# Performance work log

Hardware: AMD Instinct MI355X
Metric: run time of the kernel (lower is better)

The kernel has to match this reference:

```python
import jax, jax.numpy as jnp
import numpy as np

N = 4096          # N_TARGET_NODES (node count == feature dim)
E = 262144        # number of directed edges (avg degree 64)


def setup_inputs() -> dict:
    key = jax.random.key(0)
    k1, k2, k3, k4 = jax.random.split(key, 4)
    x = jax.random.normal(k1, (N, N), dtype=jnp.float32)
    edge_index = jax.random.randint(k2, (2, E), 0, N, dtype=jnp.int32)
    # scale weights so sigmoid inputs are O(1)
    W1 = jax.random.normal(k3, (N, N), dtype=jnp.float32) * (1.0 / np.sqrt(N))
    b1 = jnp.zeros((N,), dtype=jnp.float32)
    W2 = jax.random.normal(k4, (N, 1), dtype=jnp.float32) * (1.0 / np.sqrt(N))
    b2 = jnp.zeros((1,), dtype=jnp.float32)
    return {"x": x, "edge_index": edge_index, "W1": W1, "b1": b1, "W2": W2, "b2": b2}


def _gcn_conv(x, edge_index, W, b):
    """PyG GCNConv: h = D^{-1/2}(A+I)D^{-1/2} (x W) + b, edge weights = 1."""
    n = x.shape[0]
    h = x @ W                                   # [n, out]
    loop = jnp.arange(n, dtype=edge_index.dtype)
    src = jnp.concatenate([edge_index[0], loop])  # add self loops
    dst = jnp.concatenate([edge_index[1], loop])
    deg = jax.ops.segment_sum(jnp.ones_like(src, dtype=h.dtype), dst, num_segments=n)
    dinv = jnp.where(deg > 0, jax.lax.rsqrt(deg), 0.0)
    norm = dinv[src] * dinv[dst]                # [E+n]
    msg = h[src] * norm[:, None]                # gather + scale
    out = jax.ops.segment_sum(msg, dst, num_segments=n)  # scatter-add at targets
    return out + b


def reference(x, edge_index, W1, b1, W2, b2):
    # torch.squeeze(x) is a no-op for 2-D x
    x1 = jax.nn.sigmoid(_gcn_conv(x, edge_index, W1, b1))
    # F.dropout in eval mode is identity (deterministic reference)
    x2 = jax.nn.sigmoid(_gcn_conv(x1, edge_index, W2, b2))
    return x2  # [N, 1]
```

## Files before the change

kernel.cpp:

```cpp
#include <hip/hip_runtime.h>


typedef __attribute__((ext_vector_type(8))) short bf16x8;
typedef __attribute__((ext_vector_type(4))) float f32x4;

#define NN 4096
#define NT 64

__device__ __forceinline__ unsigned f2bf(float f) {
  unsigned u = __float_as_uint(f);
  return (u + 0x7FFFu + ((u >> 16) & 1u)) >> 16;
}

#define GLDS(g, l) __builtin_amdgcn_global_load_lds(                      \
    (const __attribute__((address_space(1))) void*)(g),                   \
    (__attribute__((address_space(3))) void*)(l), 16, 0, 0)


__global__ void init_deg_kernel(float* deg) {
  int v = blockIdx.x * 256 + threadIdx.x;
  if (v < NN) deg[v] = 1.0f;
}

__global__ void count_deg_kernel(const int* __restrict__ dst, int E, float* deg) {
  int e = blockIdx.x * 256 + threadIdx.x;
  if (e < E) atomicAdd(&deg[dst[e]], 1.0f);
}

__global__ void dinv_kernel(const float* __restrict__ deg, float* __restrict__ dinv) {
  int v = blockIdx.x * 256 + threadIdx.x;
  if (v < NN) dinv[v] = rsqrtf(deg[v]);
}

__global__ void diag_bf16_kernel(const float* __restrict__ dinv, unsigned short* __restrict__ Sbf) {
  int v = blockIdx.x * 256 + threadIdx.x;
  if (v < NN) { float d = dinv[v]; Sbf[(size_t)v * NN + v] = (unsigned short)f2bf(d * d); }
}

__global__ void scatter_bf16_kernel(const int* __restrict__ src, const int* __restrict__ dst,
                                    int E, const float* __restrict__ dinv,
                                    unsigned int* __restrict__ Sw) {
  int e = blockIdx.x * 256 + threadIdx.x;
  if (e >= E) return;
  int s = src[e], d = dst[e];
  float val = dinv[s] * dinv[d];
  size_t idx = (size_t)d * NN + s;
  unsigned int* p = Sw + (idx >> 1);
  const bool hi = (idx & 1) != 0;
  unsigned old = *p, assumed;
  do {
    assumed = old;
    unsigned short cur = hi ? (unsigned short)(assumed >> 16) : (unsigned short)(assumed & 0xFFFFu);
    float f = __uint_as_float(((unsigned)cur) << 16) + val;
    unsigned short nb = (unsigned short)f2bf(f);
    unsigned nw = hi ? ((assumed & 0x0000FFFFu) | ((unsigned)nb << 16))
                     : ((assumed & 0xFFFF0000u) | (unsigned)nb);
    old = atomicCAS(p, assumed, nw);
  } while (old != assumed);
}


__global__ void cast_kernel(const float* __restrict__ in, unsigned short* __restrict__ out, int n) {
  int i = (blockIdx.x * 256 + threadIdx.x) * 8;
  if (i >= n) return;
  const float4* p = (const float4*)(in + i);
  float4 a = p[0], b = p[1];
  uint4 o;
  o.x = f2bf(a.x) | (f2bf(a.y) << 16);
  o.y = f2bf(a.z) | (f2bf(a.w) << 16);
  o.z = f2bf(b.x) | (f2bf(b.y) << 16);
  o.w = f2bf(b.z) | (f2bf(b.w) << 16);
  *(uint4*)(out + i) = o;
}

__global__ void transpose_cast_kernel(const float* __restrict__ W, unsigned short* __restrict__ WT) {
  __shared__ float tile[64][65];
  const int tid = threadIdx.x;
  const int bx = blockIdx.x * 64, by = blockIdx.y * 64;
  const int tx = tid & 63, ty = tid >> 6;
#pragma unroll
  for (int i = 0; i < 64; i += 4)
    tile[ty + i][tx] = W[(size_t)(by + ty + i) * NN + bx + tx];
  __syncthreads();
  const int wtx = tid & 15, wty = tid >> 4;
#pragma unroll
  for (int i = 0; i < 64; i += 16) {
    int r = wty + i;
    ushort4 v;
    v.x = (unsigned short)f2bf(tile[4 * wtx + 0][r]);
    v.y = (unsigned short)f2bf(tile[4 * wtx + 1][r]);
    v.z = (unsigned short)f2bf(tile[4 * wtx + 2][r]);
    v.w = (unsigned short)f2bf(tile[4 * wtx + 3][r]);
    *(ushort4*)(WT + (size_t)(bx + r) * NN + by + 4 * wtx) = v;
  }
}


template <int EPI>
__global__ __launch_bounds__(512, 2) void gemm256_kernel(
    const unsigned short* __restrict__ A, const unsigned short* __restrict__ BT,
    unsigned short* __restrict__ C, const float* __restrict__ bias,
    const float* __restrict__ W2, float* __restrict__ h2) {
  __shared__ __align__(16) char smem[131072];
  const int tid = threadIdx.x;
  const int lane = tid & 63, wid = tid >> 6;
  const int wr = wid >> 2, wc = wid & 3;

  const int bid = blockIdx.x;
  const int swz = (bid & 7) * 32 + (bid >> 3);
  const int rowBase = (swz >> 4) * 256;
  const int colBase = (swz & 15) * 256;

  const int srow = tid >> 3;
  const int scolb = ((tid & 7) << 4) ^ ((srow & 7) << 4);
  const unsigned short* pA = A + (size_t)(rowBase + srow) * NN + (scolb >> 1);
  const unsigned short* pB = BT + (size_t)(colBase + srow) * NN + (scolb >> 1);

  const int rl = lane & 15;
  const int c0 = ((lane >> 4) << 4) ^ ((lane & 7) << 4);
  const int c1 = c0 ^ 64;
  const int aoff = (wr * 128 + rl) * 128;
  const int boff = 32768 + (wc * 64 + rl) * 128;

  f32x4 acc[8][4] = {};
  bf16x8 bk0[4], bk1[4], afA[4], afB[4];

  {
    char* w0 = smem + (wid << 10);
    GLDS(pB + (size_t)0 * 64 * NN, w0 + 32768 + 0 * 8192);
    GLDS(pB + (size_t)1 * 64 * NN, w0 + 32768 + 1 * 8192);
    GLDS(pB + (size_t)2 * 64 * NN, w0 + 32768 + 2 * 8192);
    GLDS(pB + (size_t)3 * 64 * NN, w0 + 32768 + 3 * 8192);
    GLDS(pA + (size_t)0 * 64 * NN, w0 + 0 * 8192);
    GLDS(pA + (size_t)2 * 64 * NN, w0 + 2 * 8192);
    GLDS(pA + (size_t)1 * 64 * NN, w0 + 1 * 8192);
    GLDS(pA + (size_t)3 * 64 * NN, w0 + 3 * 8192);
    asm volatile("s_waitcnt vmcnt(2)" ::: "memory");
    __builtin_amdgcn_s_barrier();
#pragma unroll
    for (int m = 0; m < 4; ++m) afA[m] = *(const bf16x8*)(smem + aoff + m * 2048 + c0);
#pragma unroll
    for (int n = 0; n < 4; ++n) bk0[n] = *(const bf16x8*)(smem + boff + n * 2048 + c0);
  }

#pragma unroll 2
  for (int t = 0; t < NT; ++t) {
    const char* lb = smem + ((t & 1) << 16);
    char* st = smem + (((t & 1) ^ 1) << 16) + (wid << 10);
    const unsigned short* s1A = pA + (size_t)(t + 1) * 64;
    const unsigned short* s1B = pB + (size_t)(t + 1) * 64;

    GLDS(s1B + (size_t)0 * 64 * NN, st + 32768 + 0 * 8192);
    GLDS(s1B + (size_t)1 * 64 * NN, st + 32768 + 1 * 8192);
    GLDS(s1B + (size_t)2 * 64 * NN, st + 32768 + 2 * 8192);
#pragma unroll
    for (int m = 0; m < 4; ++m) afB[m] = *(const bf16x8*)(lb + aoff + m * 2048 + c1);
#pragma unroll
    for (int n = 0; n < 4; ++n) bk1[n] = *(const bf16x8*)(lb + boff + n * 2048 + c1);
    __builtin_amdgcn_s_setprio(1);
#pragma unroll
    for (int m = 0; m < 4; ++m)
#pragma unroll
      for (int n = 0; n < 4; ++n)
        acc[m][n] = __builtin_amdgcn_mfma_f32_16x16x32_bf16(afA[m], bk0[n], acc[m][n], 0, 0, 0);
    __builtin_amdgcn_s_setprio(0);
    asm volatile("s_waitcnt vmcnt(3)" ::: "memory");
    __builtin_amdgcn_sched_barrier(0);

    GLDS(s1B + (size_t)3 * 64 * NN, st + 32768 + 3 * 8192);
    GLDS(s1A + (size_t)0 * 64 * NN, st + 0 * 8192);
    GLDS(s1A + (size_t)2 * 64 * NN, st + 2 * 8192);
#pragma unroll
    for (int m = 0; m < 4; ++m) afA[m] = *(const bf16x8*)(lb + aoff + (4 + m) * 2048 + c0);
    __builtin_amdgcn_s_setprio(1);
#pragma unroll
    for (int m = 0; m < 4; ++m)
#pragma unroll
      for (int n = 0; n < 4; ++n)
        acc[m][n] = __builtin_amdgcn_mfma_f32_16x16x32_bf16(afB[m], bk1[n], acc[m][n], 0, 0, 0);
    __builtin_amdgcn_s_setprio(0);
    __builtin_amdgcn_sched_barrier(0);

    GLDS(s1A + (size_t)1 * 64 * NN, st + 1 * 8192);
    GLDS(s1A + (size_t)3 * 64 * NN, st + 3 * 8192);
#pragma unroll
    for (int m = 0; m < 4; ++m) afB[m] = *(const bf16x8*)(lb + aoff + (4 + m) * 2048 + c1);
    __builtin_amdgcn_s_setprio(1);
#pragma unroll
    for (int m = 0; m < 4; ++m)
#pragma unroll
      for (int n = 0; n < 4; ++n)
        acc[4 + m][n] = __builtin_amdgcn_mfma_f32_16x16x32_bf16(afA[m], bk0[n], acc[4 + m][n], 0, 0, 0);
    __builtin_amdgcn_s_setprio(0);
    asm volatile("s_waitcnt lgkmcnt(0)" ::: "memory");
    asm volatile("s_waitcnt vmcnt(2)" ::: "memory");
    __builtin_amdgcn_s_barrier();
    __builtin_amdgcn_sched_barrier(0);

    {
      const char* nb = smem + (((t + 1) & 1) << 16);
#pragma unroll
      for (int m = 0; m < 4; ++m) afA[m] = *(const bf16x8*)(nb + aoff + m * 2048 + c0);
#pragma unroll
      for (int n = 0; n < 4; ++n) bk0[n] = *(const bf16x8*)(nb + boff + n * 2048 + c0);
    }
    __builtin_amdgcn_s_setprio(1);
#pragma unroll
    for (int m = 0; m < 4; ++m)
#pragma unroll
      for (int n = 0; n < 4; ++n)
        acc[4 + m][n] = __builtin_amdgcn_mfma_f32_16x16x32_bf16(afB[m], bk1[n], acc[4 + m][n], 0, 0, 0);
    __builtin_amdgcn_s_setprio(0);
    __builtin_amdgcn_sched_barrier(0);
  }

  const int orow = rowBase + wr * 128 + (lane >> 4) * 4;
  const int ocol = colBase + wc * 64 + (lane & 15);
  if (EPI == 0) {
#pragma unroll
    for (int n = 0; n < 4; ++n) {
      int ccol = ocol + n * 16;
#pragma unroll
      for (int m = 0; m < 8; ++m) {
#pragma unroll
        for (int i = 0; i < 4; ++i) {
          C[(size_t)(orow + m * 16 + i) * NN + ccol] = (unsigned short)f2bf(acc[m][n][i]);
        }
      }
    }
  } else {
    float bv[4], wv[4];
#pragma unroll
    for (int n = 0; n < 4; ++n) { bv[n] = bias[ocol + n * 16]; wv[n] = W2[ocol + n * 16]; }
#pragma unroll
    for (int m = 0; m < 8; ++m) {
#pragma unroll
      for (int i = 0; i < 4; ++i) {
        float s = 0.0f;
#pragma unroll
        for (int n = 0; n < 4; ++n) {
          float x = 1.0f / (1.0f + __expf(-(acc[m][n][i] + bv[n])));
          s += x * wv[n];
        }
        s += __shfl_xor(s, 1);
        s += __shfl_xor(s, 2);
        s += __shfl_xor(s, 4);
        s += __shfl_xor(s, 8);
        if ((lane & 15) == 0) atomicAdd(&h2[orow + m * 16 + i], s);
      }
    }
  }
}


__global__ void init_t_kernel(const float* __restrict__ dinv, const float* __restrict__ h2,
                              const float* __restrict__ b2, float* __restrict__ tacc) {
  int v = blockIdx.x * 256 + threadIdx.x;
  if (v < NN) tacc[v] = dinv[v] * dinv[v] * h2[v] + b2[0];
}

__global__ void scatter_t_kernel(const int* __restrict__ src, const int* __restrict__ dst,
                                 int E, const float* __restrict__ dinv,
                                 const float* __restrict__ h2, float* __restrict__ tacc) {
  int e = blockIdx.x * 256 + threadIdx.x;
  if (e < E) {
    int s = src[e], d = dst[e];
    atomicAdd(&tacc[d], dinv[s] * dinv[d] * h2[s]);
  }
}

__global__ void final_kernel(const float* __restrict__ tacc, float* __restrict__ out) {
  int v = blockIdx.x * 256 + threadIdx.x;
  if (v < NN) out[v] = 1.0f / (1.0f + __expf(-tacc[v]));
}


extern "C" void kernel_launch(void* const* d_in, const int* in_sizes, int n_in,
                              void* d_out, int out_size, void* d_ws, size_t ws_size,
                              hipStream_t stream) {
  const float* x  = (const float*)d_in[0];
  const int*   ei = (const int*)d_in[1];
  const float* W1 = (const float*)d_in[2];
  const float* b1 = (const float*)d_in[3];
  const float* W2 = (const float*)d_in[4];
  const float* b2 = (const float*)d_in[5];
  float* out = (float*)d_out;
  const int E = in_sizes[1] / 2;
  const int* esrc = ei;
  const int* edst = ei + E;

  char* w = (char*)d_ws;
  unsigned short* H1T = (unsigned short*)w;
  unsigned short* W1T = (unsigned short*)(w + (size_t)(32u << 20));
  unsigned short* Sbf = (unsigned short*)(w + (size_t)(64u << 20));
  unsigned short* Xbf = (unsigned short*)(w + (size_t)(96u << 20));
  float* deg  = (float*)(w + (size_t)(128u << 20));
  float* dinv = deg + 4096;
  float* h2   = deg + 8192;
  float* tacc = deg + 12288;

  init_deg_kernel<<<16, 256, 0, stream>>>(deg);
  count_deg_kernel<<<(E + 255) / 256, 256, 0, stream>>>(edst, E, deg);
  dinv_kernel<<<16, 256, 0, stream>>>(deg, dinv);

  hipMemsetAsync(Sbf, 0, (size_t)32 << 20, stream);
  hipMemsetAsync(h2, 0, 4096 * sizeof(float), stream);
  diag_bf16_kernel<<<16, 256, 0, stream>>>(dinv, Sbf);
  scatter_bf16_kernel<<<(E + 255) / 256, 256, 0, stream>>>(esrc, edst, E, dinv,
                                                           (unsigned int*)Sbf);

  cast_kernel<<<8192, 256, 0, stream>>>(x, Xbf, NN * NN);
  transpose_cast_kernel<<<dim3(64, 64), 256, 0, stream>>>(W1, W1T);

  gemm256_kernel<0><<<256, 512, 0, stream>>>(W1T, Xbf, H1T, nullptr, nullptr, nullptr);
  gemm256_kernel<1><<<256, 512, 0, stream>>>(Sbf, H1T, nullptr, b1, W2, h2);

  init_t_kernel<<<16, 256, 0, stream>>>(dinv, h2, b2, tacc);
  scatter_t_kernel<<<(E + 255) / 256, 256, 0, stream>>>(esrc, edst, E, dinv, h2, tacc);
  final_kernel<<<16, 256, 0, stream>>>(tacc, out);
}
```

Before: 324.8 us.

## Fuse preprocessing kernels into one launch and compute dinv on the fly

Merges the adjacency scatter, diagonal write, x cast and W1 transpose-cast into a single block-partitioned prep kernel. Replaces the dinv array with inline rsqrt of (deg+1) and folds the self-loop term and bias into the final kernel. Removes several small launches and the separate init kernels, and uses one memset for deg, h2 and tacc. The cost is extra rsqrt work per edge, plus the risk that independent stages with different resource needs now share one launch, such as the transpose path's shared-memory tile.

```diff
diff --git a/kernel.cpp b/kernel.cpp
--- a/kernel.cpp
+++ b/kernel.cpp
@@ -17,81 +17,69 @@
     (__attribute__((address_space(3))) void*)(l), 16, 0, 0)
 
 
-__global__ void init_deg_kernel(float* deg) {
-  int v = blockIdx.x * 256 + threadIdx.x;
-  if (v < NN) deg[v] = 1.0f;
-}
-
 __global__ void count_deg_kernel(const int* __restrict__ dst, int E, float* deg) {
   int e = blockIdx.x * 256 + threadIdx.x;
   if (e < E) atomicAdd(&deg[dst[e]], 1.0f);
 }
 
-__global__ void dinv_kernel(const float* __restrict__ deg, float* __restrict__ dinv) {
-  int v = blockIdx.x * 256 + threadIdx.x;
-  if (v < NN) dinv[v] = rsqrtf(deg[v]);
-}
-
-__global__ void diag_bf16_kernel(const float* __restrict__ dinv, unsigned short* __restrict__ Sbf) {
-  int v = blockIdx.x * 256 + threadIdx.x;
-  if (v < NN) { float d = dinv[v]; Sbf[(size_t)v * NN + v] = (unsigned short)f2bf(d * d); }
-}
-
-__global__ void scatter_bf16_kernel(const int* __restrict__ src, const int* __restrict__ dst,
-                                    int E, const float* __restrict__ dinv,
-                                    unsigned int* __restrict__ Sw) {
-  int e = blockIdx.x * 256 + threadIdx.x;
-  if (e >= E) return;
-  int s = src[e], d = dst[e];
-  float val = dinv[s] * dinv[d];
-  size_t idx = (size_t)d * NN + s;
-  unsigned int* p = Sw + (idx >> 1);
-  const bool hi = (idx & 1) != 0;
-  unsigned old = *p, assumed;
-  do {
-    assumed = old;
-    unsigned short cur = hi ? (unsigned short)(assumed >> 16) : (unsigned short)(assumed & 0xFFFFu);
-    float f = __uint_as_float(((unsigned)cur) << 16) + val;
-    unsigned short nb = (unsigned short)f2bf(f);
-    unsigned nw = hi ? ((assumed & 0x0000FFFFu) | ((unsigned)nb << 16))
-                     : ((assumed & 0xFFFF0000u) | (unsigned)nb);
-    old = atomicCAS(p, assumed, nw);
-  } while (old != assumed);
-}
-
-
-__global__ void cast_kernel(const float* __restrict__ in, unsigned short* __restrict__ out, int n) {
-  int i = (blockIdx.x * 256 + threadIdx.x) * 8;
-  if (i >= n) return;
-  const float4* p = (const float4*)(in + i);
-  float4 a = p[0], b = p[1];
-  uint4 o;
-  o.x = f2bf(a.x) | (f2bf(a.y) << 16);
-  o.y = f2bf(a.z) | (f2bf(a.w) << 16);
-  o.z = f2bf(b.x) | (f2bf(b.y) << 16);
-  o.w = f2bf(b.z) | (f2bf(b.w) << 16);
-  *(uint4*)(out + i) = o;
-}
-
-__global__ void transpose_cast_kernel(const float* __restrict__ W, unsigned short* __restrict__ WT) {
-  __shared__ float tile[64][65];
-  const int tid = threadIdx.x;
-  const int bx = blockIdx.x * 64, by = blockIdx.y * 64;
-  const int tx = tid & 63, ty = tid >> 6;
-#pragma unroll
-  for (int i = 0; i < 64; i += 4)
-    tile[ty + i][tx] = W[(size_t)(by + ty + i) * NN + bx + tx];
-  __syncthreads();
-  const int wtx = tid & 15, wty = tid >> 4;
-#pragma unroll
-  for (int i = 0; i < 64; i += 16) {
-    int r = wty + i;
-    ushort4 v;
-    v.x = (unsigned short)f2bf(tile[4 * wtx + 0][r]);
-    v.y = (unsigned short)f2bf(tile[4 * wtx + 1][r]);
-    v.z = (unsigned short)f2bf(tile[4 * wtx + 2][r]);
-    v.w = (unsigned short)f2bf(tile[4 * wtx + 3][r]);
-    *(ushort4*)(WT + (size_t)(bx + r) * NN + by + 4 * wtx) = v;
+
+__global__ void prep_kernel(const int* __restrict__ src, const int* __restrict__ dst, int E,
+                            const float* __restrict__ deg,
+                            unsigned int* __restrict__ Sw, unsigned short* __restrict__ Sbf,
+                            const float* __restrict__ x, unsigned short* __restrict__ Xbf,
+                            const float* __restrict__ W1, unsigned short* __restrict__ W1T) {
+  const int bid = blockIdx.x, tid = threadIdx.x;
+  if (bid < 1024) {
+    int e = bid * 256 + tid;
+    if (e >= E) return;
+    int s = src[e], d = dst[e];
+    float val = rsqrtf(deg[s] + 1.0f) * rsqrtf(deg[d] + 1.0f);
+    size_t idx = (size_t)d * NN + s;
+    unsigned int* p = Sw + (idx >> 1);
+    const bool hi = (idx & 1) != 0;
+    unsigned old = *p, assumed;
+    do {
+      assumed = old;
+      unsigned short cur = hi ? (unsigned short)(assumed >> 16) : (unsigned short)(assumed & 0xFFFFu);
+      float f = __uint_as_float(((unsigned)cur) << 16) + val;
+      unsigned short nb = (unsigned short)f2bf(f);
+      unsigned nw = hi ? ((assumed & 0x0000FFFFu) | ((unsigned)nb << 16))
+                       : ((assumed & 0xFFFF0000u) | (unsigned)nb);
+      old = atomicCAS(p, assumed, nw);
+    } while (old != assumed);
+  } else if (bid < 9216) {
+    int i = ((bid - 1024) * 256 + tid) * 8;
+    const float4* p = (const float4*)(x + i);
+    float4 a = p[0], b = p[1];
+    uint4 o;
+    o.x = f2bf(a.x) | (f2bf(a.y) << 16);
+    o.y = f2bf(a.z) | (f2bf(a.w) << 16);
+    o.z = f2bf(b.x) | (f2bf(b.y) << 16);
+    o.w = f2bf(b.z) | (f2bf(b.w) << 16);
+    *(uint4*)(Xbf + i) = o;
+  } else if (bid < 13312) {
+    __shared__ float tile[64][65];
+    const int t = bid - 9216;
+    const int bx = (t & 63) * 64, by = (t >> 6) * 64;
+    const int tx = tid & 63, ty = tid >> 6;
+#pragma unroll
+    for (int i = 0; i < 64; i += 4)
+      tile[ty + i][tx] = W1[(size_t)(by + ty + i) * NN + bx + tx];
+    __syncthreads();
+    const int wtx = tid & 15, wty = tid >> 4;
+#pragma unroll
+    for (int i = 0; i < 64; i += 16) {
+      int r = wty + i;
+      ushort4 v;
+      v.x = (unsigned short)f2bf(tile[4 * wtx + 0][r]);
+      v.y = (unsigned short)f2bf(tile[4 * wtx + 1][r]);
+      v.z = (unsigned short)f2bf(tile[4 * wtx + 2][r]);
+      v.w = (unsigned short)f2bf(tile[4 * wtx + 3][r]);
+      *(ushort4*)(W1T + (size_t)(bx + r) * NN + by + 4 * wtx) = v;
+    }
+  } else {
+    int v = (bid - 13312) * 256 + tid;
+    if (v < NN) Sbf[(size_t)v * NN + v] = (unsigned short)f2bf(1.0f / (deg[v] + 1.0f));
   }
 }
 
@@ -253,25 +241,24 @@
 }
 
 
-__global__ void init_t_kernel(const float* __restrict__ dinv, const float* __restrict__ h2,
-                              const float* __restrict__ b2, float* __restrict__ tacc) {
-  int v = blockIdx.x * 256 + threadIdx.x;
-  if (v < NN) tacc[v] = dinv[v] * dinv[v] * h2[v] + b2[0];
-}
-
 __global__ void scatter_t_kernel(const int* __restrict__ src, const int* __restrict__ dst,
-                                 int E, const float* __restrict__ dinv,
+                                 int E, const float* __restrict__ deg,
                                  const float* __restrict__ h2, float* __restrict__ tacc) {
   int e = blockIdx.x * 256 + threadIdx.x;
   if (e < E) {
     int s = src[e], d = dst[e];
-    atomicAdd(&tacc[d], dinv[s] * dinv[d] * h2[s]);
-  }
-}
-
-__global__ void final_kernel(const float* __restrict__ tacc, float* __restrict__ out) {
+    atomicAdd(&tacc[d], rsqrtf(deg[s] + 1.0f) * rsqrtf(deg[d] + 1.0f) * h2[s]);
+  }
+}
+
+__global__ void final_kernel(const float* __restrict__ tacc, const float* __restrict__ deg,
+                             const float* __restrict__ h2, const float* __restrict__ b2,
+                             float* __restrict__ out) {
   int v = blockIdx.x * 256 + threadIdx.x;
-  if (v < NN) out[v] = 1.0f / (1.0f + __expf(-tacc[v]));
+  if (v < NN) {
+    float tv = tacc[v] + h2[v] / (deg[v] + 1.0f) + b2[0];
+    out[v] = 1.0f / (1.0f + __expf(-tv));
+  }
 }
 
 
@@ -295,27 +282,20 @@
   unsigned short* Sbf = (unsigned short*)(w + (size_t)(64u << 20));
   unsigned short* Xbf = (unsigned short*)(w + (size_t)(96u << 20));
   float* deg  = (float*)(w + (size_t)(128u << 20));
-  float* dinv = deg + 4096;
-  float* h2   = deg + 8192;
-  float* tacc = deg + 12288;
-
-  init_deg_kernel<<<16, 256, 0, stream>>>(deg);
+  float* h2   = deg + 4096;
+  float* tacc = deg + 8192;
+
+  hipMemsetAsync(deg, 0, 3 * 4096 * sizeof(float), stream);
+  hipMemsetAsync(Sbf, 0, (size_t)32 << 20, stream);
+
   count_deg_kernel<<<(E + 255) / 256, 256, 0, stream>>>(edst, E, deg);
-  dinv_kernel<<<16, 256, 0, stream>>>(deg, dinv);
-
-  hipMemsetAsync(Sbf, 0, (size_t)32 << 20, stream);
-  hipMemsetAsync(h2, 0, 4096 * sizeof(float), stream);
-  diag_bf16_kernel<<<16, 256, 0, stream>>>(dinv, Sbf);
-  scatter_bf16_kernel<<<(E + 255) / 256, 256, 0, stream>>>(esrc, edst, E, dinv,
-                                                           (unsigned int*)Sbf);
-
-  cast_kernel<<<8192, 256, 0, stream>>>(x, Xbf, NN * NN);
-  transpose_cast_kernel<<<dim3(64, 64), 256, 0, stream>>>(W1, W1T);
+
+  prep_kernel<<<13328, 256, 0, stream>>>(esrc, edst, E, deg, (unsigned int*)Sbf, Sbf,
+                                         x, Xbf, W1, W1T);
 
   gemm256_kernel<0><<<256, 512, 0, stream>>>(W1T, Xbf, H1T, nullptr, nullptr, nullptr);
   gemm256_kernel<1><<<256, 512, 0, stream>>>(Sbf, H1T, nullptr, b1, W2, h2);
 
-  init_t_kernel<<<16, 256, 0, stream>>>(dinv, h2, b2, tacc);
-  scatter_t_kernel<<<(E + 255) / 256, 256, 0, stream>>>(esrc, edst, E, dinv, h2, tacc);
-  final_kernel<<<16, 256, 0, stream>>>(tacc, out);
-}
+  scatter_t_kernel<<<(E + 255) / 256, 256, 0, stream>>>(esrc, edst, E, deg, h2, tacc);
+  final_kernel<<<16, 256, 0, stream>>>(tacc, deg, h2, b2, out);
+}
```

Result: faster. 311.2 us (-4.2%).
